# Performance work log

Hardware: AMD Instinct MI355X
Metric: run time of the kernel (lower is better)

The kernel has to match this reference:

```python
import jax, jax.numpy as jnp
import numpy as np

N_NODES = 20000
N_EDGES = 320000
N_GRAPHS = 64
OBS = 64
EDGE_DIM = 16
HEADS = 4
HID = 64
NEG_SLOPE = 0.2
EPS = 1e-16


def _gat_layer(x, src, dst, edge_attr, W, We, att_src, att_dst, att_edge, b):
    """PyG GATConv (concat=True, eval mode: no dropout).
    x: [N, Fin], edge_attr: [E, De], W: [Fin, H*C], We: [De, H*C],
    att_*: [H, C], b: [H*C]. Returns [N, H*C]."""
    N = x.shape[0]
    h = (x @ W).reshape(N, HEADS, HID)                      # [N,H,C]
    he = (edge_attr @ We).reshape(-1, HEADS, HID)           # [E,H,C]
    a_src = jnp.einsum('nhc,hc->nh', h, att_src)            # [N,H]
    a_dst = jnp.einsum('nhc,hc->nh', h, att_dst)
    a_e = jnp.einsum('ehc,hc->eh', he, att_edge)            # [E,H]
    alpha = a_src[src] + a_dst[dst] + a_e                   # [E,H]
    alpha = jax.nn.leaky_relu(alpha, NEG_SLOPE)
    # segment softmax over destination neighborhoods
    m = jax.ops.segment_max(alpha, dst, num_segments=N)     # [N,H]
    m = jnp.where(jnp.isfinite(m), m, 0.0)
    ea = jnp.exp(alpha - m[dst])
    denom = jax.ops.segment_sum(ea, dst, num_segments=N)    # [N,H]
    alpha = ea / (denom[dst] + EPS)
    msg = h[src] * alpha[:, :, None]                        # [E,H,C]
    out = jax.ops.segment_sum(msg, dst, num_segments=N)     # [N,H,C]
    return out.reshape(N, HEADS * HID) + b


def _make_params(key):
    ks = jax.random.split(key, 18)
    p = {}
    dims_in = [OBS, HEADS * HID, HEADS * HID]
    for i in range(3):
        j = i * 6
        fin = dims_in[i]
        p[f'W{i+1}'] = jax.random.normal(ks[j], (fin, HEADS * HID), jnp.float32) * (1.0 / np.sqrt(fin))
        p[f'We{i+1}'] = jax.random.normal(ks[j+1], (EDGE_DIM, HEADS * HID), jnp.float32) * (1.0 / np.sqrt(EDGE_DIM))
        p[f'att_src{i+1}'] = jax.random.normal(ks[j+2], (HEADS, HID), jnp.float32) * 0.1
        p[f'att_dst{i+1}'] = jax.random.normal(ks[j+3], (HEADS, HID), jnp.float32) * 0.1
        p[f'att_edge{i+1}'] = jax.random.normal(ks[j+4], (HEADS, HID), jnp.float32) * 0.1
        p[f'b{i+1}'] = jnp.zeros((HEADS * HID,), jnp.float32)
    return p


def setup_inputs() -> dict:
    key = jax.random.key(0)
    k1, k2, k3, k4, kp = jax.random.split(key, 5)
    inp = {
        'x': jax.random.normal(k1, (N_NODES, OBS), jnp.float32),
        'edge_index': jax.random.randint(k2, (2, N_EDGES), 0, N_NODES, jnp.int64),
        'edge_attr': jax.random.normal(k3, (N_EDGES, EDGE_DIM), jnp.float32),
        'batch': jnp.sort(jax.random.randint(k4, (N_NODES,), 0, N_GRAPHS, jnp.int64)),
    }
    inp.update(_make_params(kp))
    return inp


def reference(x, edge_index, edge_attr, batch,
              W1, We1, att_src1, att_dst1, att_edge1, b1,
              W2, We2, att_src2, att_dst2, att_edge2, b2,
              W3, We3, att_src3, att_dst3, att_edge3, b3):
    src, dst = edge_index[0], edge_index[1]
    h = jax.nn.relu(_gat_layer(x, src, dst, edge_attr, W1, We1, att_src1, att_dst1, att_edge1, b1))
    h = jax.nn.relu(_gat_layer(h, src, dst, edge_attr, W2, We2, att_src2, att_dst2, att_edge2, b2))
    h = jax.nn.relu(_gat_layer(h, src, dst, edge_attr, W3, We3, att_src3, att_dst3, att_edge3, b3))
    # global mean pool over graphs
    sums = jax.ops.segment_sum(h, batch, num_segments=N_GRAPHS)      # [G, H*C]
    counts = jax.ops.segment_sum(jnp.ones((h.shape[0], 1), h.dtype), batch, num_segments=N_GRAPHS)
    pooled = sums / jnp.maximum(counts, 1.0)
    return jnp.tanh(pooled)
```

## Files before the change

kernel.cpp:

```cpp
#include <hip/hip_runtime.h>
#include <hip/hip_bf16.h>
#include <hip/hip_fp16.h>
#include <math.h>

#define N_NODES 20000
#define N_EDGES 320000
#define N_GRAPHS 64
#define OBS 64
#define EDGE_DIM 16
#define HEADS 4
#define HID 64
#define HC 256
#define NEG_SLOPE 0.2f
#define EPSF 1e-16f
#define N_SCAN_BLOCKS ((N_NODES + 255) / 256)
#define CVT_BLOCKS (N_NODES * OBS / 4 / 256)
#define CAP 64

typedef _Float16 f16x8 __attribute__((ext_vector_type(8)));
typedef float f32x4 __attribute__((ext_vector_type(4)));

#define SB_ZERO  N_SCAN_BLOCKS
#define SB_CVT   (SB_ZERO + CVT_BLOCKS)
#define SB_WT0   (SB_CVT + OBS)
#define SB_WT1   (SB_WT0 + HC)
#define SB_WT2   (SB_WT1 + HC)
#define SB_TOT   (SB_WT2 + 3)
__global__ __launch_bounds__(256) void setup_kernel(int* __restrict__ counts,
                                                    float* __restrict__ pooled,
                                                    int* __restrict__ gcounts,
                                                    const float* __restrict__ x, __half* __restrict__ x16,
                                                    const float* __restrict__ W0, const float* __restrict__ W1,
                                                    const float* __restrict__ W2,
                                                    __half* __restrict__ wt0, __half* __restrict__ wt1,
                                                    __half* __restrict__ wt2,
                                                    const float* __restrict__ We0, const float* __restrict__ ae0,
                                                    const float* __restrict__ We1, const float* __restrict__ ae1,
                                                    const float* __restrict__ We2, const float* __restrict__ ae2,
                                                    float* __restrict__ w_eff3) {
    int b = blockIdx.x, t = threadIdx.x;
    if (b < SB_ZERO) {
        int i = b * 256 + t;
        if (i < N_NODES) counts[i] = 0;
        if (i < N_GRAPHS * HC) pooled[i] = 0.f;
        if (i < N_GRAPHS) gcounts[i] = 0;
    } else if (b < SB_CVT) {
        int i = ((b - SB_ZERO) * 256 + t) * 4;
        float4 v = *(const float4*)(x + i);
        *(__half2*)(x16 + i)     = __floats2half2_rn(v.x, v.y);
        *(__half2*)(x16 + i + 2) = __floats2half2_rn(v.z, v.w);
    } else if (b < SB_WT0) {
        int k = b - SB_CVT;
        wt0[(size_t)t * OBS + k] = __float2half(W0[(size_t)k * HC + t]);
    } else if (b < SB_WT1) {
        int k = b - SB_WT0;
        wt1[(size_t)t * HC + k] = __float2half(W1[(size_t)k * HC + t]);
    } else if (b < SB_WT2) {
        int k = b - SB_WT1;
        wt2[(size_t)t * HC + k] = __float2half(W2[(size_t)k * HC + t]);
    } else {
        int l = b - SB_WT2;
        if (t >= 64) return;
        const float* We = (l == 0) ? We0 : (l == 1) ? We1 : We2;
        const float* ae = (l == 0) ? ae0 : (l == 1) ? ae1 : ae2;
        int hh = t >> 4, d = t & 15;
        float acc = 0.f;
        #pragma unroll 8
        for (int c = 0; c < HID; ++c)
            acc += We[d * HC + hh * HID + c] * ae[hh * HID + c];
        w_eff3[l * 64 + hh * 16 + d] = acc;
    }
}

__global__ __launch_bounds__(256) void count_kernel(const int* __restrict__ ei, int* __restrict__ counts) {
    int e = blockIdx.x * 256 + threadIdx.x;
    if (e >= N_EDGES) return;
    atomicAdd(&counts[ei[N_EDGES + e]], 1);
}

__global__ __launch_bounds__(256) void scan_local_kernel(const int* __restrict__ counts,
                                                         int* __restrict__ row_start,
                                                         int* __restrict__ blk_tot) {
    int b = blockIdx.x, t = threadIdx.x;
    int i = b * 256 + t;
    int v = (i < N_NODES) ? counts[i] : 0;
    int lane = t & 63, w = t >> 6;
    int x = v;
    #pragma unroll
    for (int off = 1; off < 64; off <<= 1) {
        int y = __shfl_up(x, off, 64);
        if (lane >= off) x += y;
    }
    __shared__ int wsum[4];
    __shared__ int woff[4];
    if (lane == 63) wsum[w] = x;
    __syncthreads();
    if (t == 0) {
        int s = 0;
        #pragma unroll
        for (int k = 0; k < 4; ++k) { woff[k] = s; s += wsum[k]; }
        blk_tot[b] = s;
    }
    __syncthreads();
    if (i < N_NODES) row_start[i] = x - v + woff[w];
}

__global__ __launch_bounds__(256) void scan_add_kernel(int* __restrict__ row_start,
                                                       const int* __restrict__ blk_tot,
                                                       int* __restrict__ cursor) {
    __shared__ int sd[128];
    int b = blockIdx.x, t = threadIdx.x;
    if (t < 128) sd[t] = (t < b && t < N_SCAN_BLOCKS) ? blk_tot[t] : 0;
    __syncthreads();
    #pragma unroll
    for (int off = 64; off >= 1; off >>= 1) {
        if (t < off) sd[t] += sd[t + off];
        __syncthreads();
    }
    int base = sd[0];
    int i = b * 256 + t;
    if (i < N_NODES) {
        int r = row_start[i] + base;
        row_start[i] = r;
        cursor[i] = r;
    }
}

__global__ __launch_bounds__(256) void fill_ae_kernel(const int* __restrict__ ei,
                                                      const float* __restrict__ edge_attr,
                                                      const float* __restrict__ w_eff3,
                                                      int* __restrict__ cursor,
                                                      int* __restrict__ src_csr,
                                                      float4* __restrict__ ae_csr) {
    __shared__ float wsh[192];
    int t = threadIdx.x;
    if (t < 192) wsh[t] = w_eff3[t];
    __syncthreads();
    int e = blockIdx.x * 256 + t;
    if (e >= N_EDGES) return;
    int s = ei[e];
    int d = ei[N_EDGES + e];
    int pos = atomicAdd(&cursor[d], 1);
    src_csr[pos] = s;
    const float* ea = edge_attr + (size_t)e * EDGE_DIM;
    float x[16];
    #pragma unroll
    for (int i = 0; i < 16; i += 4) {
        float4 v = *(const float4*)(ea + i);
        x[i] = v.x; x[i + 1] = v.y; x[i + 2] = v.z; x[i + 3] = v.w;
    }
    #pragma unroll
    for (int l = 0; l < 3; ++l) {
        float al[4];
        #pragma unroll
        for (int hh = 0; hh < 4; ++hh) {
            float acc = 0.f;
            #pragma unroll
            for (int i = 0; i < 16; ++i) acc += x[i] * wsh[l * 64 + hh * 16 + i];
            al[hh] = acc;
        }
        ae_csr[(size_t)l * N_EDGES + pos] = make_float4(al[0], al[1], al[2], al[3]);
    }
}

template <int NKT>
__global__ __launch_bounds__(256) void gemm16_kernel(const __half* __restrict__ A16,
                                                     const __half* __restrict__ Wt16,
                                                     __half* __restrict__ C16, int M,
                                                     const float* __restrict__ att_src,
                                                     const float* __restrict__ att_dst,
                                                     float* __restrict__ a_src,
                                                     float* __restrict__ a_dst) {
    constexpr int K = NKT * 32;
    __shared__ __align__(16) _Float16 lds[64 * 264];
    int t = threadIdx.x;
    int w = t >> 6, l = t & 63;
    int cg = l & 15, gg = l >> 4;
    int m0 = blockIdx.x * 64;

    {
        int row = (t >> 6) * 16 + (t & 15);
        int k8 = (t >> 4) & 3;
        int rg = m0 + row;
        if (rg >= M) rg = M - 1;
        const _Float16* ag = (const _Float16*)A16 + (size_t)rg * K + k8 * 8;
        f16x8 tmp[NKT];
        #pragma unroll
        for (int j = 0; j < NKT; ++j) tmp[j] = *(const f16x8*)(ag + j * 32);
        #pragma unroll
        for (int j = 0; j < NKT; ++j) *(f16x8*)&lds[(size_t)(j * 256 + t) * 8] = tmp[j];
    }
    __syncthreads();

    f32x4 acc[4][4] = {};
    const _Float16* bg = (const _Float16*)Wt16 + (size_t)(w * 64 + cg) * K + gg * 8;
    #pragma unroll 2
    for (int kt = 0; kt < NKT; ++kt) {
        f16x8 bf[4], af[4];
        #pragma unroll
        for (int ni = 0; ni < 4; ++ni)
            bf[ni] = *(const f16x8*)(bg + (size_t)(ni * 16) * K + kt * 32);
        #pragma unroll
        for (int mi = 0; mi < 4; ++mi)
            af[mi] = *(const f16x8*)&lds[(size_t)(kt * 256 + mi * 64 + l) * 8];
        #pragma unroll
        for (int mi = 0; mi < 4; ++mi)
            #pragma unroll
            for (int ni = 0; ni < 4; ++ni)
                acc[mi][ni] = __builtin_amdgcn_mfma_f32_16x16x32_f16(af[mi], bf[ni], acc[mi][ni], 0, 0, 0);
    }

    {
        float avs[4], avd[4];
        #pragma unroll
        for (int ni = 0; ni < 4; ++ni) {
            avs[ni] = att_src[w * 64 + ni * 16 + cg];
            avd[ni] = att_dst[w * 64 + ni * 16 + cg];
        }
        #pragma unroll
        for (int mi = 0; mi < 4; ++mi)
            #pragma unroll
            for (int reg = 0; reg < 4; ++reg) {
                float ps = acc[mi][0][reg] * avs[0] + acc[mi][1][reg] * avs[1]
                         + acc[mi][2][reg] * avs[2] + acc[mi][3][reg] * avs[3];
                float pd = acc[mi][0][reg] * avd[0] + acc[mi][1][reg] * avd[1]
                         + acc[mi][2][reg] * avd[2] + acc[mi][3][reg] * avd[3];
                #pragma unroll
                for (int o = 1; o < 16; o <<= 1) {
                    ps += __shfl_xor(ps, o, 64);
                    pd += __shfl_xor(pd, o, 64);
                }
                int m = m0 + mi * 16 + gg * 4 + reg;
                if (cg == 0 && m < M) {
                    a_src[(size_t)m * 4 + w] = ps;
                    a_dst[(size_t)m * 4 + w] = pd;
                }
            }
    }

    __syncthreads();
    #pragma unroll
    for (int mi = 0; mi < 4; ++mi)
        #pragma unroll
        for (int ni = 0; ni < 4; ++ni)
            #pragma unroll
            for (int reg = 0; reg < 4; ++reg) {
                int row = mi * 16 + gg * 4 + reg;
                int col = w * 64 + ni * 16 + cg;
                lds[row * 264 + col] = (_Float16)acc[mi][ni][reg];
            }
    __syncthreads();
    #pragma unroll
    for (int i = 0; i < 8; ++i) {
        int g = i * 256 + t;
        int row = g >> 5, cw = g & 31;
        int m = m0 + row;
        if (m < M) {
            f16x8 v = *(const f16x8*)&lds[row * 264 + cw * 8];
            *(f16x8*)((_Float16*)C16 + (size_t)m * HC + cw * 8) = v;
        }
    }
}

__global__ __launch_bounds__(256) void aggregate5_kernel(const int* __restrict__ src_csr,
                                                         const float4* __restrict__ ae_csr,
                                                         const int* __restrict__ row_start,
                                                         const int* __restrict__ counts,
                                                         const float* __restrict__ a_src,
                                                         const float* __restrict__ a_dst,
                                                         const __half* __restrict__ h16,
                                                         const float* __restrict__ bias,
                                                         __half* __restrict__ out16) {
    __shared__ float wlds[4][4][CAP + 1];
    int wid = threadIdx.x >> 6, lane = threadIdx.x & 63;
    int n = blockIdx.x * 4 + wid;
    int start = row_start[n];
    int deg = counts[n];
    const float4* ae = ae_csr + start;
    const int* sp = src_csr + start;
    float4 ad = *(const float4*)(a_dst + (size_t)n * 4);

    float d0 = 0.f, d1 = 0.f, d2 = 0.f, d3 = 0.f;
    for (int i = lane; i < deg; i += 64) {
        float4 a = ae[i];
        int s = sp[i];
        float4 as = *(const float4*)(a_src + (size_t)s * 4);
        float v0 = a.x + as.x + ad.x; v0 = v0 > 0.f ? v0 : NEG_SLOPE * v0;
        float v1 = a.y + as.y + ad.y; v1 = v1 > 0.f ? v1 : NEG_SLOPE * v1;
        float v2 = a.z + as.z + ad.z; v2 = v2 > 0.f ? v2 : NEG_SLOPE * v2;
        float v3 = a.w + as.w + ad.w; v3 = v3 > 0.f ? v3 : NEG_SLOPE * v3;
        float e0 = __expf(v0);
        float e1 = __expf(v1);
        float e2 = __expf(v2);
        float e3 = __expf(v3);
        d0 += e0; d1 += e1; d2 += e2; d3 += e3;
        if (i < CAP) {
            wlds[wid][0][i] = e0; wlds[wid][1][i] = e1;
            wlds[wid][2][i] = e2; wlds[wid][3][i] = e3;
        }
    }
    #pragma unroll
    for (int o = 32; o > 0; o >>= 1) {
        d0 += __shfl_xor(d0, o, 64);
        d1 += __shfl_xor(d1, o, 64);
        d2 += __shfl_xor(d2, o, 64);
        d3 += __shfl_xor(d3, o, 64);
    }

    int g = lane >> 5, j = lane & 31;
    int head = j >> 3;
    float dh = (head < 2) ? (head == 0 ? d0 : d1) : (head == 2 ? d2 : d3);
    float adh = (head < 2) ? (head == 0 ? ad.x : ad.y) : (head == 2 ? ad.z : ad.w);

    float acc[8] = {};
    int niter = (deg + 1) >> 1;
    if (deg <= CAP) {
        int it = 0;
        for (; it + 4 <= niter; it += 4) {
            int s_[4]; float w_[4]; f16x8 hv_[4];
            #pragma unroll
            for (int u = 0; u < 4; ++u) {
                int e = (it + u) * 2 + g;
                bool valid = e < deg;
                int ec = valid ? e : deg - 1;
                s_[u] = sp[ec];
                float wv = wlds[wid][head][ec];
                w_[u] = valid ? wv : 0.f;
            }
            #pragma unroll
            for (int u = 0; u < 4; ++u)
                hv_[u] = *(const f16x8*)((const _Float16*)h16 + (size_t)s_[u] * HC + j * 8);
            #pragma unroll
            for (int u = 0; u < 4; ++u)
                #pragma unroll
                for (int q = 0; q < 8; ++q) acc[q] += w_[u] * (float)hv_[u][q];
        }
        for (; it < niter; ++it) {
            int e = it * 2 + g;
            bool valid = e < deg;
            int ec = valid ? e : deg - 1;
            int s = sp[ec];
            float wv = wlds[wid][head][ec];
            float wgt = valid ? wv : 0.f;
            f16x8 hv = *(const f16x8*)((const _Float16*)h16 + (size_t)s * HC + j * 8);
            #pragma unroll
            for (int q = 0; q < 8; ++q) acc[q] += wgt * (float)hv[q];
        }
    } else {
        for (int it = 0; it < niter; ++it) {
            int e = it * 2 + g;
            bool valid = e < deg;
            int ec = valid ? e : deg - 1;
            int s = sp[ec];
            float wgt;
            if (ec < CAP) {
                wgt = wlds[wid][head][ec];
            } else {
                float4 a = ae[ec];
                float aa = (head < 2) ? (head == 0 ? a.x : a.y) : (head == 2 ? a.z : a.w);
                const float* asp = a_src + (size_t)s * 4;
                float v = aa + asp[head] + adh;
                v = v > 0.f ? v : NEG_SLOPE * v;
                wgt = __expf(v);
            }
            if (!valid) wgt = 0.f;
            f16x8 hv = *(const f16x8*)((const _Float16*)h16 + (size_t)s * HC + j * 8);
            #pragma unroll
            for (int q = 0; q < 8; ++q) acc[q] += wgt * (float)hv[q];
        }
    }
    #pragma unroll
    for (int q = 0; q < 8; ++q) acc[q] += __shfl_xor(acc[q], 32, 64);

    if (g == 0) {
        float invd = 1.f / (dh + EPSF);
        float4 b0 = *(const float4*)(bias + j * 8);
        float4 b1 = *(const float4*)(bias + j * 8 + 4);
        float r[8];
        r[0] = fmaxf(acc[0] * invd + b0.x, 0.f);
        r[1] = fmaxf(acc[1] * invd + b0.y, 0.f);
        r[2] = fmaxf(acc[2] * invd + b0.z, 0.f);
        r[3] = fmaxf(acc[3] * invd + b0.w, 0.f);
        r[4] = fmaxf(acc[4] * invd + b1.x, 0.f);
        r[5] = fmaxf(acc[5] * invd + b1.y, 0.f);
        r[6] = fmaxf(acc[6] * invd + b1.z, 0.f);
        r[7] = fmaxf(acc[7] * invd + b1.w, 0.f);
        f16x8 o;
        #pragma unroll
        for (int q = 0; q < 8; ++q) o[q] = (_Float16)r[q];
        *(f16x8*)((_Float16*)out16 + (size_t)n * HC + j * 8) = o;
    }
}

#define NPB 100
__global__ __launch_bounds__(256) void pool_kernel(const __half* __restrict__ h,
                                                   const int* __restrict__ batch,
                                                   float* __restrict__ pooled,
                                                   int* __restrict__ gcounts) {
    int t = threadIdx.x;
    int n0 = blockIdx.x * NPB;
    int n1 = n0 + NPB;
    if (n1 > N_NODES) n1 = N_NODES;
    if (n0 >= N_NODES) return;
    int cur = batch[n0];
    float acc = 0.f;
    int cnt = 0;
    for (int n = n0; n < n1; ++n) {
        int g = batch[n];
        if (g != cur) {
            atomicAdd(&pooled[cur * HC + t], acc);
            if (t == 0) atomicAdd(&gcounts[cur], cnt);
            acc = 0.f; cnt = 0; cur = g;
        }
        acc += __half2float(h[(size_t)n * HC + t]);
        cnt++;
    }
    atomicAdd(&pooled[cur * HC + t], acc);
    if (t == 0) atomicAdd(&gcounts[cur], cnt);
}

__global__ __launch_bounds__(256) void finalize_kernel(const float* __restrict__ pooled,
                                                       const int* __restrict__ gcounts,
                                                       float* __restrict__ out) {
    int g = blockIdx.x, t = threadIdx.x;
    float c = (float)(gcounts[g] > 1 ? gcounts[g] : 1);
    out[g * HC + t] = tanhf(pooled[g * HC + t] / c);
}

extern "C" void kernel_launch(void* const* d_in, const int* in_sizes, int n_in,
                              void* d_out, int out_size, void* d_ws, size_t ws_size,
                              hipStream_t stream) {
    const float* x         = (const float*)d_in[0];
    const int*   ei        = (const int*)d_in[1];
    const float* edge_attr = (const float*)d_in[2];
    const int*   batch     = (const int*)d_in[3];
    const float* Wl[3]  = {(const float*)d_in[4],  (const float*)d_in[10], (const float*)d_in[16]};
    const float* Wel[3] = {(const float*)d_in[5],  (const float*)d_in[11], (const float*)d_in[17]};
    const float* asl[3] = {(const float*)d_in[6],  (const float*)d_in[12], (const float*)d_in[18]};
    const float* adl[3] = {(const float*)d_in[7],  (const float*)d_in[13], (const float*)d_in[19]};
    const float* ael[3] = {(const float*)d_in[8],  (const float*)d_in[14], (const float*)d_in[20]};
    const float* bl[3]  = {(const float*)d_in[9],  (const float*)d_in[15], (const float*)d_in[21]};
    float* out = (float*)d_out;

    char* p = (char*)d_ws;
    auto alloc = [&](size_t bytes) -> void* {
        void* r = (void*)p;
        p += (bytes + 255) & ~(size_t)255;
        return r;
    };
    __half* x16       = (__half*)alloc((size_t)N_NODES * OBS * 2);
    __half* hA16      = (__half*)alloc((size_t)N_NODES * HC * 2);
    __half* hB16      = (__half*)alloc((size_t)N_NODES * HC * 2);
    __half* wt0       = (__half*)alloc((size_t)HC * OBS * 2);
    __half* wt1       = (__half*)alloc((size_t)HC * HC * 2);
    __half* wt2       = (__half*)alloc((size_t)HC * HC * 2);
    float* a_src      = (float*)alloc((size_t)N_NODES * 4 * 4);
    float* a_dst      = (float*)alloc((size_t)N_NODES * 4 * 4);
    float4* ae_csr    = (float4*)alloc((size_t)3 * N_EDGES * 16);
    int* counts       = (int*)alloc((size_t)N_NODES * 4);
    int* row_start    = (int*)alloc((size_t)N_NODES * 4);
    int* cursor       = (int*)alloc((size_t)N_NODES * 4);
    int* src_csr      = (int*)alloc((size_t)N_EDGES * 4);
    float* w_eff3     = (float*)alloc(192 * 4);
    float* pooled     = (float*)alloc((size_t)N_GRAPHS * HC * 4);
    int* gcounts      = (int*)alloc((size_t)N_GRAPHS * 4);
    int* blk_tot      = (int*)alloc((size_t)N_SCAN_BLOCKS * 4);

    setup_kernel<<<SB_TOT, 256, 0, stream>>>(counts, pooled, gcounts, x, x16,
                                             Wl[0], Wl[1], Wl[2], wt0, wt1, wt2,
                                             Wel[0], ael[0], Wel[1], ael[1], Wel[2], ael[2],
                                             w_eff3);

    count_kernel<<<N_EDGES / 256, 256, 0, stream>>>(ei, counts);
    scan_local_kernel<<<N_SCAN_BLOCKS, 256, 0, stream>>>(counts, row_start, blk_tot);
    scan_add_kernel<<<N_SCAN_BLOCKS, 256, 0, stream>>>(row_start, blk_tot, cursor);
    fill_ae_kernel<<<N_EDGES / 256, 256, 0, stream>>>(ei, edge_attr, w_eff3, cursor,
                                                      src_csr, ae_csr);

    const int ngrid = (N_NODES + 63) / 64;
    const __half* wtl[3] = {wt0, wt1, wt2};
    const __half* cur_in = x16;
    for (int l = 0; l < 3; ++l) {
        if (l == 0)
            gemm16_kernel<2><<<ngrid, 256, 0, stream>>>(cur_in, wtl[l], hA16, N_NODES,
                                                        asl[l], adl[l], a_src, a_dst);
        else
            gemm16_kernel<8><<<ngrid, 256, 0, stream>>>(cur_in, wtl[l], hA16, N_NODES,
                                                        asl[l], adl[l], a_src, a_dst);
        aggregate5_kernel<<<N_NODES / 4, 256, 0, stream>>>(src_csr, ae_csr + (size_t)l * N_EDGES,
                                                           row_start, counts, a_src, a_dst,
                                                           hA16, bl[l], hB16);
        cur_in = hB16;
    }

    pool_kernel<<<(N_NODES + NPB - 1) / NPB, 256, 0, stream>>>(hB16, batch, pooled, gcounts);
    finalize_kernel<<<N_GRAPHS, 256, 0, stream>>>(pooled, gcounts, out);
}
```

Before: 221.3 us.

## Split aggregation across two waves per node and fuse pooling with finalize

The aggregation kernel now uses two 64-lane waves per destination node, each covering half the channels (two heads). Within a wave, four edges are processed concurrently rather than two, which raises parallelism per node and shortens the gather loop. Both waves recompute the softmax denominators redundantly. Separately, the atomic pool and finalize kernels are replaced by one kernel per graph that binary-searches the sorted batch array and sums its node range serially. This drops the zero-init and atomics but leaves only 64 blocks doing long serial loops.

```diff
diff --git a/kernel.cpp b/kernel.cpp
--- a/kernel.cpp
+++ b/kernel.cpp
@@ -27,8 +27,6 @@
 #define SB_WT2   (SB_WT1 + HC)
 #define SB_TOT   (SB_WT2 + 3)
 __global__ __launch_bounds__(256) void setup_kernel(int* __restrict__ counts,
-                                                    float* __restrict__ pooled,
-                                                    int* __restrict__ gcounts,
                                                     const float* __restrict__ x, __half* __restrict__ x16,
                                                     const float* __restrict__ W0, const float* __restrict__ W1,
                                                     const float* __restrict__ W2,
@@ -42,8 +40,6 @@
     if (b < SB_ZERO) {
         int i = b * 256 + t;
         if (i < N_NODES) counts[i] = 0;
-        if (i < N_GRAPHS * HC) pooled[i] = 0.f;
-        if (i < N_GRAPHS) gcounts[i] = 0;
     } else if (b < SB_CVT) {
         int i = ((b - SB_ZERO) * 256 + t) * 4;
         float4 v = *(const float4*)(x + i);
@@ -262,7 +258,7 @@
     }
 }
 
-__global__ __launch_bounds__(256) void aggregate5_kernel(const int* __restrict__ src_csr,
+__global__ __launch_bounds__(512) void aggregate6_kernel(const int* __restrict__ src_csr,
                                                          const float4* __restrict__ ae_csr,
                                                          const int* __restrict__ row_start,
                                                          const int* __restrict__ counts,
@@ -271,9 +267,10 @@
                                                          const __half* __restrict__ h16,
                                                          const float* __restrict__ bias,
                                                          __half* __restrict__ out16) {
-    __shared__ float wlds[4][4][CAP + 1];
-    int wid = threadIdx.x >> 6, lane = threadIdx.x & 63;
-    int n = blockIdx.x * 4 + wid;
+    __shared__ float wlds[8][4][CAP + 1];
+    int wid2 = threadIdx.x >> 6, lane = threadIdx.x & 63;
+    int nw = wid2 >> 1, half = wid2 & 1;
+    int n = blockIdx.x * 4 + nw;
     int start = row_start[n];
     int deg = counts[n];
     const float4* ae = ae_csr + start;
@@ -295,8 +292,8 @@
         float e3 = __expf(v3);
         d0 += e0; d1 += e1; d2 += e2; d3 += e3;
         if (i < CAP) {
-            wlds[wid][0][i] = e0; wlds[wid][1][i] = e1;
-            wlds[wid][2][i] = e2; wlds[wid][3][i] = e3;
+            wlds[wid2][0][i] = e0; wlds[wid2][1][i] = e1;
+            wlds[wid2][2][i] = e2; wlds[wid2][3][i] = e3;
         }
     }
     #pragma unroll
@@ -307,75 +304,79 @@
         d3 += __shfl_xor(d3, o, 64);
     }
 
-    int g = lane >> 5, j = lane & 31;
-    int head = j >> 3;
-    float dh = (head < 2) ? (head == 0 ? d0 : d1) : (head == 2 ? d2 : d3);
-    float adh = (head < 2) ? (head == 0 ? ad.x : ad.y) : (head == 2 ? ad.z : ad.w);
+    int g = lane >> 4, j = lane & 15;
+    int head = half * 2 + (j >> 3);
+    int cbase = half * 128 + j * 8;
+    float dh = (head == 0) ? d0 : (head == 1) ? d1 : (head == 2) ? d2 : d3;
+    float adh = (head == 0) ? ad.x : (head == 1) ? ad.y : (head == 2) ? ad.z : ad.w;
 
     float acc[8] = {};
-    int niter = (deg + 1) >> 1;
+    int niter = (deg + 3) >> 2;
     if (deg <= CAP) {
         int it = 0;
-        for (; it + 4 <= niter; it += 4) {
-            int s_[4]; float w_[4]; f16x8 hv_[4];
-            #pragma unroll
-            for (int u = 0; u < 4; ++u) {
-                int e = (it + u) * 2 + g;
+        for (; it + 2 <= niter; it += 2) {
+            int s_[2]; float w_[2]; f16x8 hv_[2];
+            #pragma unroll
+            for (int u = 0; u < 2; ++u) {
+                int e = (it + u) * 4 + g;
                 bool valid = e < deg;
                 int ec = valid ? e : deg - 1;
                 s_[u] = sp[ec];
-                float wv = wlds[wid][head][ec];
+                float wv = wlds[wid2][head][ec];
                 w_[u] = valid ? wv : 0.f;
             }
             #pragma unroll
-            for (int u = 0; u < 4; ++u)
-                hv_[u] = *(const f16x8*)((const _Float16*)h16 + (size_t)s_[u] * HC + j * 8);
-            #pragma unroll
-            for (int u = 0; u < 4; ++u)
+            for (int u = 0; u < 2; ++u)
+                hv_[u] = *(const f16x8*)((const _Float16*)h16 + (size_t)s_[u] * HC + cbase);
+            #pragma unroll
+            for (int u = 0; u < 2; ++u)
                 #pragma unroll
                 for (int q = 0; q < 8; ++q) acc[q] += w_[u] * (float)hv_[u][q];
         }
         for (; it < niter; ++it) {
-            int e = it * 2 + g;
+            int e = it * 4 + g;
             bool valid = e < deg;
             int ec = valid ? e : deg - 1;
             int s = sp[ec];
-            float wv = wlds[wid][head][ec];
+            float wv = wlds[wid2][head][ec];
             float wgt = valid ? wv : 0.f;
-            f16x8 hv = *(const f16x8*)((const _Float16*)h16 + (size_t)s * HC + j * 8);
+            f16x8 hv = *(const f16x8*)((const _Float16*)h16 + (size_t)s * HC + cbase);
             #pragma unroll
             for (int q = 0; q < 8; ++q) acc[q] += wgt * (float)hv[q];
         }
     } else {
         for (int it = 0; it < niter; ++it) {
-            int e = it * 2 + g;
+            int e = it * 4 + g;
             bool valid = e < deg;
             int ec = valid ? e : deg - 1;
             int s = sp[ec];
             float wgt;
             if (ec < CAP) {
-                wgt = wlds[wid][head][ec];
+                wgt = wlds[wid2][head][ec];
             } else {
                 float4 a = ae[ec];
-                float aa = (head < 2) ? (head == 0 ? a.x : a.y) : (head == 2 ? a.z : a.w);
+                float aa = (head == 0) ? a.x : (head == 1) ? a.y : (head == 2) ? a.z : a.w;
                 const float* asp = a_src + (size_t)s * 4;
                 float v = aa + asp[head] + adh;
                 v = v > 0.f ? v : NEG_SLOPE * v;
                 wgt = __expf(v);
             }
             if (!valid) wgt = 0.f;
-            f16x8 hv = *(const f16x8*)((const _Float16*)h16 + (size_t)s * HC + j * 8);
+            f16x8 hv = *(const f16x8*)((const _Float16*)h16 + (size_t)s * HC + cbase);
             #pragma unroll
             for (int q = 0; q < 8; ++q) acc[q] += wgt * (float)hv[q];
         }
     }
     #pragma unroll
-    for (int q = 0; q < 8; ++q) acc[q] += __shfl_xor(acc[q], 32, 64);
+    for (int q = 0; q < 8; ++q) {
+        acc[q] += __shfl_xor(acc[q], 16, 64);
+        acc[q] += __shfl_xor(acc[q], 32, 64);
+    }
 
     if (g == 0) {
         float invd = 1.f / (dh + EPSF);
-        float4 b0 = *(const float4*)(bias + j * 8);
-        float4 b1 = *(const float4*)(bias + j * 8 + 4);
+        float4 b0 = *(const float4*)(bias + cbase);
+        float4 b1 = *(const float4*)(bias + cbase + 4);
         float r[8];
         r[0] = fmaxf(acc[0] * invd + b0.x, 0.f);
         r[1] = fmaxf(acc[1] * invd + b0.y, 0.f);
@@ -388,43 +389,26 @@
         f16x8 o;
         #pragma unroll
         for (int q = 0; q < 8; ++q) o[q] = (_Float16)r[q];
-        *(f16x8*)((_Float16*)out16 + (size_t)n * HC + j * 8) = o;
-    }
-}
-
-#define NPB 100
-__global__ __launch_bounds__(256) void pool_kernel(const __half* __restrict__ h,
-                                                   const int* __restrict__ batch,
-                                                   float* __restrict__ pooled,
-                                                   int* __restrict__ gcounts) {
-    int t = threadIdx.x;
-    int n0 = blockIdx.x * NPB;
-    int n1 = n0 + NPB;
-    if (n1 > N_NODES) n1 = N_NODES;
-    if (n0 >= N_NODES) return;
-    int cur = batch[n0];
+        *(f16x8*)((_Float16*)out16 + (size_t)n * HC + cbase) = o;
+    }
+}
+
+__global__ __launch_bounds__(256) void pool2_kernel(const __half* __restrict__ h,
+                                                    const int* __restrict__ batch,
+                                                    float* __restrict__ out) {
+    int g = blockIdx.x, t = threadIdx.x;
+    int a = 0, b = N_NODES;
+    while (a < b) { int m = (a + b) >> 1; if (batch[m] < g) a = m + 1; else b = m; }
+    int lo = a;
+    b = N_NODES;
+    while (a < b) { int m = (a + b) >> 1; if (batch[m] < g + 1) a = m + 1; else b = m; }
+    int hi = a;
     float acc = 0.f;
-    int cnt = 0;
-    for (int n = n0; n < n1; ++n) {
-        int g = batch[n];
-        if (g != cur) {
-            atomicAdd(&pooled[cur * HC + t], acc);
-            if (t == 0) atomicAdd(&gcounts[cur], cnt);
-            acc = 0.f; cnt = 0; cur = g;
-        }
+    for (int n = lo; n < hi; ++n)
         acc += __half2float(h[(size_t)n * HC + t]);
-        cnt++;
-    }
-    atomicAdd(&pooled[cur * HC + t], acc);
-    if (t == 0) atomicAdd(&gcounts[cur], cnt);
-}
-
-__global__ __launch_bounds__(256) void finalize_kernel(const float* __restrict__ pooled,
-                                                       const int* __restrict__ gcounts,
-                                                       float* __restrict__ out) {
-    int g = blockIdx.x, t = threadIdx.x;
-    float c = (float)(gcounts[g] > 1 ? gcounts[g] : 1);
-    out[g * HC + t] = tanhf(pooled[g * HC + t] / c);
+    int cnt = hi - lo;
+    float c = (cnt > 1) ? (float)cnt : 1.f;
+    out[(size_t)g * HC + t] = tanhf(acc / c);
 }
 
 extern "C" void kernel_launch(void* const* d_in, const int* in_sizes, int n_in,
@@ -462,11 +446,9 @@
     int* cursor       = (int*)alloc((size_t)N_NODES * 4);
     int* src_csr      = (int*)alloc((size_t)N_EDGES * 4);
     float* w_eff3     = (float*)alloc(192 * 4);
-    float* pooled     = (float*)alloc((size_t)N_GRAPHS * HC * 4);
-    int* gcounts      = (int*)alloc((size_t)N_GRAPHS * 4);
     int* blk_tot      = (int*)alloc((size_t)N_SCAN_BLOCKS * 4);
 
-    setup_kernel<<<SB_TOT, 256, 0, stream>>>(counts, pooled, gcounts, x, x16,
+    setup_kernel<<<SB_TOT, 256, 0, stream>>>(counts, x, x16,
                                              Wl[0], Wl[1], Wl[2], wt0, wt1, wt2,
                                              Wel[0], ael[0], Wel[1], ael[1], Wel[2], ael[2],
                                              w_eff3);
@@ -487,12 +469,11 @@
         else
             gemm16_kernel<8><<<ngrid, 256, 0, stream>>>(cur_in, wtl[l], hA16, N_NODES,
                                                         asl[l], adl[l], a_src, a_dst);
-        aggregate5_kernel<<<N_NODES / 4, 256, 0, stream>>>(src_csr, ae_csr + (size_t)l * N_EDGES,
+        aggregate6_kernel<<<N_NODES / 4, 512, 0, stream>>>(src_csr, ae_csr + (size_t)l * N_EDGES,
                                                            row_start, counts, a_src, a_dst,
                                                            hA16, bl[l], hB16);
         cur_in = hB16;
     }
 
-    pool_kernel<<<(N_NODES + NPB - 1) / NPB, 256, 0, stream>>>(hB16, batch, pooled, gcounts);
-    finalize_kernel<<<N_GRAPHS, 256, 0, stream>>>(pooled, gcounts, out);
-}
+    pool2_kernel<<<N_GRAPHS, 256, 0, stream>>>(hB16, batch, out);
+}
```

New measurement: 298.3 us. 1.35x slower.
